# Kernel optimization log

Measured on AMD Instinct MI355X. Metric: run time of the kernel, lower is better.

## Reference

```python
import jax, jax.numpy as jnp
import numpy as np

NF = 512      # nfeatures (input == hidden size)
NL = 3        # nlabels
T = 32768     # sequence length (unbatched)
EPS = 1e-5


def _lstm_layer(x, w_ih, w_hh, b_ih, b_hh):
    # x: [T, F_in]; w_ih: [4H, F_in]; w_hh: [4H, H]
    H = w_hh.shape[1]
    xg = x @ w_ih.T + (b_ih + b_hh)  # precompute input gates: [T, 4H]

    def step(carry, xg_t):
        h, c = carry
        g = xg_t + h @ w_hh.T
        i, f, gc, o = jnp.split(g, 4)
        i = jax.nn.sigmoid(i)
        f = jax.nn.sigmoid(f)
        gc = jnp.tanh(gc)
        o = jax.nn.sigmoid(o)
        c = f * c + i * gc
        h = o * jnp.tanh(c)
        return (h, c), h

    h0 = jnp.zeros((H,), x.dtype)
    _, hs = jax.lax.scan(step, (h0, h0), xg)
    return hs  # [T, H]


def _bn(x, gamma, beta):
    # training-mode BatchNorm1d over the batch (time) axis, biased variance
    m = x.mean(0)
    v = x.var(0)
    return (x - m) * jax.lax.rsqrt(v + EPS) * gamma + beta


def setup_inputs() -> dict:
    key = jax.random.key(0)
    ks = jax.random.split(key, 16)
    s = 1.0 / np.sqrt(NF)
    u = lambda k, shp, sc: jax.random.uniform(k, shp, jnp.float32, -sc, sc)
    inp = {"x": jax.random.normal(ks[0], (T, NF), jnp.float32)}
    # LSTM layer 0 and 1 (input = hidden = NF)
    inp["w_ih0"] = u(ks[1], (4 * NF, NF), s); inp["w_hh0"] = u(ks[2], (4 * NF, NF), s)
    inp["b_ih0"] = u(ks[3], (4 * NF,), s);   inp["b_hh0"] = u(ks[4], (4 * NF,), s)
    inp["w_ih1"] = u(ks[5], (4 * NF, NF), s); inp["w_hh1"] = u(ks[6], (4 * NF, NF), s)
    inp["b_ih1"] = u(ks[7], (4 * NF,), s);   inp["b_hh1"] = u(ks[8], (4 * NF,), s)
    # MLP head
    inp["w1"] = u(ks[9], (128, NF), s);  inp["b1"] = u(ks[9], (128,), s)
    inp["g1"] = jnp.ones((128,), jnp.float32); inp["beta1"] = jnp.zeros((128,), jnp.float32)
    s2 = 1.0 / np.sqrt(128)
    inp["w2"] = u(ks[10], (64, 128), s2); inp["b2"] = u(ks[10], (64,), s2)
    inp["g2"] = jnp.ones((64,), jnp.float32); inp["beta2"] = jnp.zeros((64,), jnp.float32)
    s3 = 1.0 / np.sqrt(64)
    inp["w3"] = u(ks[11], (NL, 64), s3); inp["b3"] = u(ks[11], (NL,), s3)
    return inp


def reference(x, w_ih0, w_hh0, b_ih0, b_hh0, w_ih1, w_hh1, b_ih1, b_hh1,
              w1, b1, g1, beta1, w2, b2, g2, beta2, w3, b3):
    h = _lstm_layer(x, w_ih0, w_hh0, b_ih0, b_hh0)
    h = _lstm_layer(h, w_ih1, w_hh1, b_ih1, b_hh1)
    h = _bn(jax.nn.relu(h @ w1.T + b1), g1, beta1)
    h = _bn(jax.nn.relu(h @ w2.T + b2), g2, beta2)
    return h @ w3.T + b3  # [T, NL]


if __name__ == "__main__":
    out = reference(**setup_inputs())
    print(out.shape, out.dtype)
```

## Files before the change

### kernel.cpp

```cpp
#include <hip/hip_runtime.h>
#include <stdint.h>

#define TSEQ 32768
#define HDIM 512
#define NWGL 64
#define DPW  8
#define POISON32 0x7FA55A5Au

__device__ __forceinline__ float sigf(float x){ return 1.f/(1.f+__expf(-x)); }
__device__ __forceinline__ float tanhf_fast(float x){ return 1.f - 2.f/(1.f+__expf(2.f*x)); }

__device__ __forceinline__ uint32_t agload(uint32_t* p){
  return __hip_atomic_load(p, __ATOMIC_RELAXED, __HIP_MEMORY_SCOPE_AGENT);
}
__device__ __forceinline__ void agstore(uint32_t* p, uint32_t v){
  __hip_atomic_store(p, v, __ATOMIC_RELAXED, __HIP_MEMORY_SCOPE_AGENT);
}

__global__ __launch_bounds__(256,1)
void poison_kernel(uint64_t* __restrict__ a, uint64_t* __restrict__ b, int n64){
  const uint64_t P = (((uint64_t)POISON32)<<32) | (uint64_t)POISON32;
  int i = blockIdx.x*256 + threadIdx.x;
  const int st = gridDim.x*256;
  for (; i < n64; i += st){
    __hip_atomic_store(a+i, P, __ATOMIC_RELAXED, __HIP_MEMORY_SCOPE_AGENT);
    __hip_atomic_store(b+i, P, __ATOMIC_RELAXED, __HIP_MEMORY_SCOPE_AGENT);
  }
}

__global__ __launch_bounds__(256,1)
void lstm_persistent(const float* __restrict__ x,
                     const float* __restrict__ wih0, const float* __restrict__ whh0,
                     const float* __restrict__ bih0, const float* __restrict__ bhh0,
                     const float* __restrict__ wih1, const float* __restrict__ whh1,
                     const float* __restrict__ bih1, const float* __restrict__ bhh1,
                     float* __restrict__ hs0, float* __restrict__ hs1)
{
  const int wg    = blockIdx.x;
  const int layer = (wg >= NWGL) ? 1 : 0;
  const int wgl   = layer ? wg - NWGL : wg;
  const int tid   = threadIdx.x;
  const int r     = tid & 31;
  const int c     = tid >> 5;

  const float* Wih = layer ? wih1 : wih0;
  const float* Whh = layer ? whh1 : whh0;
  float* dst = layer ? hs1 : hs0;

  const int grow = (r>>3)*HDIM + wgl*DPW + (r&7);

  float4 wi[16], wr[16];
  #pragma unroll
  for (int q=0;q<16;q++){
    wi[q] = *(const float4*)&Wih[(size_t)grow*HDIM + c*64 + q*4];
    wr[q] = *(const float4*)&Whh[(size_t)grow*HDIM + c*64 + q*4];
  }
  float bias = 0.f;
  if (tid < 32) bias = (layer?bih1:bih0)[grow] + (layer?bhh1:bhh0)[grow];

  float cstate = 0.f;

  __shared__ float ha[HDIM];
  __shared__ float hr[HDIM];
  __shared__ float part[128];
  __shared__ float gl[32];

  float4 xpref = make_float4(0.f,0.f,0.f,0.f);
  if (!layer && tid >= 128) xpref = *(const float4*)&x[(tid-128)*4];

  #pragma unroll 1
  for (int t = 0; t < TSEQ; ++t){
    if (!layer && tid >= 128) *(float4*)&ha[(tid-128)*4] = xpref;

    if (t > 0 && tid < 128){
      uint32_t* p = (uint32_t*)(dst + (size_t)(t-1)*HDIM) + tid*4;
      uint32_t v0,v1,v2,v3;
      do {
        v0 = agload(p+0); v1 = agload(p+1); v2 = agload(p+2); v3 = agload(p+3);
      } while ((v0==POISON32)|(v1==POISON32)|(v2==POISON32)|(v3==POISON32));
      float4 f; f.x=__uint_as_float(v0); f.y=__uint_as_float(v1);
                f.z=__uint_as_float(v2); f.w=__uint_as_float(v3);
      *(float4*)&hr[tid*4] = f;
    }
    if (layer && tid >= 128){
      uint32_t* p = (uint32_t*)(hs0 + (size_t)t*HDIM) + (tid-128)*4;
      uint32_t v0,v1,v2,v3;
      do {
        v0 = agload(p+0); v1 = agload(p+1); v2 = agload(p+2); v3 = agload(p+3);
      } while ((v0==POISON32)|(v1==POISON32)|(v2==POISON32)|(v3==POISON32));
      float4 f; f.x=__uint_as_float(v0); f.y=__uint_as_float(v1);
                f.z=__uint_as_float(v2); f.w=__uint_as_float(v3);
      *(float4*)&ha[(tid-128)*4] = f;
    }
    if (t == 0 && tid < 128) *(float4*)&hr[tid*4] = make_float4(0.f,0.f,0.f,0.f);
    __syncthreads();

    if (!layer && tid >= 128 && (t+1) < TSEQ)
      xpref = *(const float4*)&x[(size_t)(t+1)*HDIM + (tid-128)*4];

    float s0=0.f,s1=0.f,s2=0.f,s3=0.f;
    const float4* hr4 = (const float4*)(hr + c*64);
    const float4* ha4 = (const float4*)(ha + c*64);
    #pragma unroll
    for (int q=0;q<16;q++){
      float4 hv = hr4[q];
      s0 = fmaf(wr[q].x, hv.x, s0); s1 = fmaf(wr[q].y, hv.y, s1);
      s2 = fmaf(wr[q].z, hv.z, s2); s3 = fmaf(wr[q].w, hv.w, s3);
      float4 av = ha4[q];
      s0 = fmaf(wi[q].x, av.x, s0); s1 = fmaf(wi[q].y, av.y, s1);
      s2 = fmaf(wi[q].z, av.z, s2); s3 = fmaf(wi[q].w, av.w, s3);
    }
    float acc = (s0+s1)+(s2+s3);
    acc += __shfl_xor(acc, 32);
    if ((tid & 63) < 32) part[(tid>>6)*32 + (tid&31)] = acc;
    __syncthreads();
    if (tid < 32) gl[tid] = part[tid] + part[32+tid] + part[64+tid] + part[96+tid] + bias;
    __syncthreads();
    if (tid < 8){
      float gi = sigf(gl[tid]);
      float gf = sigf(gl[8+tid]);
      float gg = tanhf_fast(gl[16+tid]);
      float go = sigf(gl[24+tid]);
      cstate = fmaf(gf, cstate, gi*gg);
      float h = go * tanhf_fast(cstate);
      agstore((uint32_t*)(dst + (size_t)t*HDIM + wgl*DPW + tid), __float_as_uint(h));
    }
  }
}

__global__ __launch_bounds__(256)
void transpose_kernel(const float* __restrict__ w1, const float* __restrict__ w2,
                      float* __restrict__ w1t, float* __restrict__ w2t){
  int i = blockIdx.x*256 + threadIdx.x;
  if (i < 128*512){ int rr = i >> 9, k = i & 511; w1t[k*128 + rr] = w1[i]; }
  if (i < 64*128){ int rr = i >> 7, k = i & 127; w2t[k*64 + rr] = w2[i]; }
}

__global__ __launch_bounds__(128)
void mlp1_kernel(const float* __restrict__ hs1, const float* __restrict__ w1t,
                 const float* __restrict__ b1, float* __restrict__ z1){
  __shared__ float hsl[2048];
  const int tid = threadIdx.x;
  const size_t row0 = (size_t)blockIdx.x*4;
  #pragma unroll
  for (int q=0;q<4;q++){
    int idx = tid + q*128;
    *(float4*)&hsl[idx*4] = *(const float4*)&hs1[row0*512 + idx*4];
  }
  __syncthreads();
  float a0=0.f,a1=0.f,a2=0.f,a3=0.f;
  #pragma unroll 4
  for (int k=0;k<512;k++){
    float wv = w1t[k*128 + tid];
    a0 = fmaf(wv, hsl[k],      a0);
    a1 = fmaf(wv, hsl[512+k],  a1);
    a2 = fmaf(wv, hsl[1024+k], a2);
    a3 = fmaf(wv, hsl[1536+k], a3);
  }
  float bb = b1[tid];
  z1[(row0+0)*128 + tid] = fmaxf(a0+bb, 0.f);
  z1[(row0+1)*128 + tid] = fmaxf(a1+bb, 0.f);
  z1[(row0+2)*128 + tid] = fmaxf(a2+bb, 0.f);
  z1[(row0+3)*128 + tid] = fmaxf(a3+bb, 0.f);
}

template<int NF_>
__global__ void stats_partial(const float* __restrict__ z, float* __restrict__ part){
  const int cf = threadIdx.x;
  const int b  = blockIdx.x;
  float s=0.f, sq=0.f;
  const float* p = z + (size_t)b*512*NF_ + cf;
  for (int rr=0; rr<512; rr++){
    float v = p[(size_t)rr*NF_];
    s += v; sq = fmaf(v, v, sq);
  }
  part[(b*NF_ + cf)*2+0] = s;
  part[(b*NF_ + cf)*2+1] = sq;
}

template<int NF_>
__global__ void stats_final(const float* __restrict__ part, const float* __restrict__ gamma,
                            const float* __restrict__ beta, float* __restrict__ sc,
                            float* __restrict__ sh){
  const int cf = threadIdx.x;
  float s=0.f, sq=0.f;
  for (int b=0;b<64;b++){ s += part[(b*NF_+cf)*2]; sq += part[(b*NF_+cf)*2+1]; }
  const float inv = 1.f/32768.f;
  float m = s*inv;
  float v = fmaf(sq, inv, -m*m);
  float scale = gamma[cf]*rsqrtf(v + 1e-5f);
  sc[cf] = scale;
  sh[cf] = fmaf(-m, scale, beta[cf]);
}

__global__ __launch_bounds__(64)
void mlp2_kernel(const float* __restrict__ z1, const float* __restrict__ w2t,
                 const float* __restrict__ b2, const float* __restrict__ sc1,
                 const float* __restrict__ sh1, float* __restrict__ z2){
  __shared__ float zl[1024];
  const int tid = threadIdx.x;
  const size_t row0 = (size_t)blockIdx.x*8;
  #pragma unroll
  for (int q=0;q<4;q++){
    int idx = tid + q*64;
    float4 v = *(const float4*)&z1[row0*128 + idx*4];
    int k0 = (idx*4) & 127;
    v.x = fmaf(v.x, sc1[k0+0], sh1[k0+0]);
    v.y = fmaf(v.y, sc1[k0+1], sh1[k0+1]);
    v.z = fmaf(v.z, sc1[k0+2], sh1[k0+2]);
    v.w = fmaf(v.w, sc1[k0+3], sh1[k0+3]);
    *(float4*)&zl[idx*4] = v;
  }
  __syncthreads();
  float acc[8] = {0.f,0.f,0.f,0.f,0.f,0.f,0.f,0.f};
  #pragma unroll 4
  for (int k=0;k<128;k++){
    float wv = w2t[k*64 + tid];
    #pragma unroll
    for (int rr=0;rr<8;rr++) acc[rr] = fmaf(wv, zl[rr*128 + k], acc[rr]);
  }
  float bb = b2[tid];
  #pragma unroll
  for (int rr=0;rr<8;rr++)
    z2[(row0+rr)*64 + tid] = fmaxf(acc[rr]+bb, 0.f);
}

__global__ __launch_bounds__(256)
void mlp3_kernel(const float* __restrict__ z2, const float* __restrict__ w3,
                 const float* __restrict__ b3, const float* __restrict__ sc2,
                 const float* __restrict__ sh2, float* __restrict__ out){
  const int tid = threadIdx.x;
  const int lane = tid & 63;
  const size_t row = (size_t)blockIdx.x*4 + (tid>>6);
  float v = fmaf(z2[row*64 + lane], sc2[lane], sh2[lane]);
  float p0 = v*w3[lane], p1 = v*w3[64+lane], p2 = v*w3[128+lane];
  #pragma unroll
  for (int off=32; off; off>>=1){
    p0 += __shfl_xor(p0, off);
    p1 += __shfl_xor(p1, off);
    p2 += __shfl_xor(p2, off);
  }
  if (lane == 0){
    out[row*3+0] = p0 + b3[0];
    out[row*3+1] = p1 + b3[1];
    out[row*3+2] = p2 + b3[2];
  }
}

extern "C" void kernel_launch(void* const* d_in, const int* in_sizes, int n_in,
                              void* d_out, int out_size, void* d_ws, size_t ws_size,
                              hipStream_t stream){
  (void)in_sizes; (void)n_in; (void)out_size;
  const float* x    = (const float*)d_in[0];
  const float* wih0 = (const float*)d_in[1];
  const float* whh0 = (const float*)d_in[2];
  const float* bih0 = (const float*)d_in[3];
  const float* bhh0 = (const float*)d_in[4];
  const float* wih1 = (const float*)d_in[5];
  const float* whh1 = (const float*)d_in[6];
  const float* bih1 = (const float*)d_in[7];
  const float* bhh1 = (const float*)d_in[8];
  const float* w1   = (const float*)d_in[9];
  const float* b1   = (const float*)d_in[10];
  const float* g1   = (const float*)d_in[11];
  const float* be1  = (const float*)d_in[12];
  const float* w2   = (const float*)d_in[13];
  const float* b2   = (const float*)d_in[14];
  const float* g2   = (const float*)d_in[15];
  const float* be2  = (const float*)d_in[16];
  const float* w3   = (const float*)d_in[17];
  const float* b3   = (const float*)d_in[18];
  float* ws  = (float*)d_ws;
  float* out = (float*)d_out;

  if (ws_size < (size_t)33554432ull*4ull) return;

  float* hs0  = ws;
  float* hs1  = ws + 16777216;
  float* z1    = ws;
  float* z2    = ws + 4194304;
  float* w1t   = ws + 6291456;
  float* w2t   = ws + 6356992;
  float* part1 = ws + 6365184;
  float* part2 = ws + 6381568;
  float* sc1   = ws + 6389760;
  float* sh1   = sc1 + 128;
  float* sc2   = sh1 + 128;
  float* sh2   = sc2 + 64;

  poison_kernel<<<1024, 256, 0, stream>>>((uint64_t*)hs0, (uint64_t*)hs1, 8388608);
  lstm_persistent<<<128, 256, 0, stream>>>(x, wih0, whh0, bih0, bhh0,
                                           wih1, whh1, bih1, bhh1, hs0, hs1);
  transpose_kernel<<<256, 256, 0, stream>>>(w1, w2, w1t, w2t);
  mlp1_kernel<<<8192, 128, 0, stream>>>(hs1, w1t, b1, z1);
  stats_partial<128><<<64, 128, 0, stream>>>(z1, part1);
  stats_final<128><<<1, 128, 0, stream>>>(part1, g1, be1, sc1, sh1);
  mlp2_kernel<<<4096, 64, 0, stream>>>(z1, w2t, b2, sc1, sh1, z2);
  stats_partial<64><<<64, 64, 0, stream>>>(z2, part2);
  stats_final<64><<<1, 64, 0, stream>>>(part2, g2, be2, sc2, sh2);
  mlp3_kernel<<<8192, 256, 0, stream>>>(z2, w3, b3, sc2, sh2, out);
}
```

Measured before the change: 75.66 ms.

## Restructure persistent LSTM: 512-thread WGs, bf16 hidden exchange, shuffle gate reduction

Halves the LSTM workgroup count to 32 per layer with 512 threads each, 16 hidden units per workgroup. Hidden states are exchanged between workgroups as packed bf16 pairs through 64-bit atomic polls, and the gate reduction moves from LDS passes to wave shuffles. Double-buffered, swizzled LDS lets the input-weight matvec overlap the recurrent poll. This cuts per-step barriers and inter-CU traffic on the latency-bound recurrence, but rounding hidden states to bf16 lowers precision through both layers and into the MLP head.

```diff
diff --git a/kernel.cpp b/kernel.cpp
--- a/kernel.cpp
+++ b/kernel.cpp
@@ -3,127 +3,176 @@
 
 #define TSEQ 32768
 #define HDIM 512
-#define NWGL 64
-#define DPW  8
-#define POISON32 0x7FA55A5Au
+#define NWGL 32
+#define WGT  512
+#define DPW  16
+#define POISON32 0x7FA57FA5u
+
+typedef float f4 __attribute__((ext_vector_type(4)));
 
 __device__ __forceinline__ float sigf(float x){ return 1.f/(1.f+__expf(-x)); }
 __device__ __forceinline__ float tanhf_fast(float x){ return 1.f - 2.f/(1.f+__expf(2.f*x)); }
 
-__device__ __forceinline__ uint32_t agload(uint32_t* p){
+__device__ __forceinline__ uint64_t agload64(const uint64_t* p){
   return __hip_atomic_load(p, __ATOMIC_RELAXED, __HIP_MEMORY_SCOPE_AGENT);
 }
-__device__ __forceinline__ void agstore(uint32_t* p, uint32_t v){
+__device__ __forceinline__ void agstore32(uint32_t* p, uint32_t v){
   __hip_atomic_store(p, v, __ATOMIC_RELAXED, __HIP_MEMORY_SCOPE_AGENT);
 }
+__device__ __forceinline__ uint32_t f2bf(float f){
+  uint32_t u = __float_as_uint(f);
+  u += 0x7fffu + ((u>>16)&1u);
+  return u>>16;
+}
+__device__ __forceinline__ bool pois(uint64_t v){
+  return (((uint32_t)v)==POISON32) | (((uint32_t)(v>>32))==POISON32);
+}
+__device__ __forceinline__ void unpack_store(uint64_t v, float* buf, int gsw){
+  uint32_t aa = (uint32_t)v, bb = (uint32_t)(v>>32);
+  float4 f;
+  f.x = __uint_as_float(aa<<16);
+  f.y = __uint_as_float(aa & 0xffff0000u);
+  f.z = __uint_as_float(bb<<16);
+  f.w = __uint_as_float(bb & 0xffff0000u);
+  *(float4*)&buf[gsw*4] = f;
+}
+__device__ __forceinline__ f4 ntload(const float* p){
+  return __builtin_nontemporal_load((const f4*)p);
+}
+
+#define PIN4(v) asm volatile("" : "+v"((v).x), "+v"((v).y), "+v"((v).z), "+v"((v).w))
+#define PINS do { _Pragma("unroll") for (int _q=0;_q<16;_q++){ PIN4(wi[_q]); PIN4(wr[_q]); } } while(0)
+
+#define MV(bufptr, W) do { \
+  const float* _b = (bufptr); \
+  _Pragma("unroll") \
+  for (int q=0;q<16;q++){ \
+    float4 hv = *(const float4*)&_b[(((c<<4)|((q^c)&15))<<2)]; \
+    s0 = fmaf(W[q].x, hv.x, s0); s1 = fmaf(W[q].y, hv.y, s1); \
+    s2 = fmaf(W[q].z, hv.z, s2); s3 = fmaf(W[q].w, hv.w, s3); } \
+} while(0)
+
+#define REDUCE_GATES_PUBLISH(dstp) do { \
+  float s = (s0+s1)+(s2+s3); \
+  s += __shfl_xor(s,1); s += __shfl_xor(s,2); s += __shfl_xor(s,4); \
+  s += bias; \
+  float fv = __shfl_down(s,8), gv = __shfl_down(s,16), ov = __shfl_down(s,24); \
+  float gi = sigf(s), gf = sigf(fv), gg = tanhf_fast(gv), go = sigf(ov); \
+  cst = fmaf(gf, cst, gi*gg); \
+  float h = go * tanhf_fast(cst); \
+  float ho = __shfl(h, 32); \
+  if (lane == 0) agstore32((dstp) + (size_t)t*256 + wgl*8 + w, f2bf(h) | (f2bf(ho)<<16)); \
+} while(0)
 
 __global__ __launch_bounds__(256,1)
-void poison_kernel(uint64_t* __restrict__ a, uint64_t* __restrict__ b, int n64){
-  const uint64_t P = (((uint64_t)POISON32)<<32) | (uint64_t)POISON32;
+void poison_kernel(uint64_t* __restrict__ a, int n64){
+  const uint64_t P = 0x7FA57FA57FA57FA5ull;
   int i = blockIdx.x*256 + threadIdx.x;
   const int st = gridDim.x*256;
-  for (; i < n64; i += st){
+  for (; i < n64; i += st)
     __hip_atomic_store(a+i, P, __ATOMIC_RELAXED, __HIP_MEMORY_SCOPE_AGENT);
-    __hip_atomic_store(b+i, P, __ATOMIC_RELAXED, __HIP_MEMORY_SCOPE_AGENT);
-  }
-}
-
-__global__ __launch_bounds__(256,1)
+}
+
+__global__ __launch_bounds__(WGT, 2)
 void lstm_persistent(const float* __restrict__ x,
                      const float* __restrict__ wih0, const float* __restrict__ whh0,
                      const float* __restrict__ bih0, const float* __restrict__ bhh0,
                      const float* __restrict__ wih1, const float* __restrict__ whh1,
                      const float* __restrict__ bih1, const float* __restrict__ bhh1,
-                     float* __restrict__ hs0, float* __restrict__ hs1)
+                     uint32_t* __restrict__ hs0u, uint32_t* __restrict__ hs1u)
 {
   const int wg    = blockIdx.x;
   const int layer = (wg >= NWGL) ? 1 : 0;
   const int wgl   = layer ? wg - NWGL : wg;
   const int tid   = threadIdx.x;
-  const int r     = tid & 31;
-  const int c     = tid >> 5;
+  const int w     = tid >> 6;
+  const int lane  = tid & 63;
+  const int rl    = lane >> 3;
+  const int c     = lane & 7;
+  const int g     = rl & 3;
+  const int dd    = rl >> 2;
+  const int grow  = g*HDIM + wgl*DPW + 2*w + dd;
 
   const float* Wih = layer ? wih1 : wih0;
   const float* Whh = layer ? whh1 : whh0;
-  float* dst = layer ? hs1 : hs0;
-
-  const int grow = (r>>3)*HDIM + wgl*DPW + (r&7);
+  const float bias = (layer?bih1:bih0)[grow] + (layer?bhh1:bhh0)[grow];
 
   float4 wi[16], wr[16];
-  #pragma unroll
-  for (int q=0;q<16;q++){
-    wi[q] = *(const float4*)&Wih[(size_t)grow*HDIM + c*64 + q*4];
-    wr[q] = *(const float4*)&Whh[(size_t)grow*HDIM + c*64 + q*4];
-  }
-  float bias = 0.f;
-  if (tid < 32) bias = (layer?bih1:bih0)[grow] + (layer?bhh1:bhh0)[grow];
-
-  float cstate = 0.f;
-
-  __shared__ float ha[HDIM];
-  __shared__ float hr[HDIM];
-  __shared__ float part[128];
-  __shared__ float gl[32];
-
-  float4 xpref = make_float4(0.f,0.f,0.f,0.f);
-  if (!layer && tid >= 128) xpref = *(const float4*)&x[(tid-128)*4];
-
-  #pragma unroll 1
-  for (int t = 0; t < TSEQ; ++t){
-    if (!layer && tid >= 128) *(float4*)&ha[(tid-128)*4] = xpref;
-
-    if (t > 0 && tid < 128){
-      uint32_t* p = (uint32_t*)(dst + (size_t)(t-1)*HDIM) + tid*4;
-      uint32_t v0,v1,v2,v3;
-      do {
-        v0 = agload(p+0); v1 = agload(p+1); v2 = agload(p+2); v3 = agload(p+3);
-      } while ((v0==POISON32)|(v1==POISON32)|(v2==POISON32)|(v3==POISON32));
-      float4 f; f.x=__uint_as_float(v0); f.y=__uint_as_float(v1);
-                f.z=__uint_as_float(v2); f.w=__uint_as_float(v3);
-      *(float4*)&hr[tid*4] = f;
-    }
-    if (layer && tid >= 128){
-      uint32_t* p = (uint32_t*)(hs0 + (size_t)t*HDIM) + (tid-128)*4;
-      uint32_t v0,v1,v2,v3;
-      do {
-        v0 = agload(p+0); v1 = agload(p+1); v2 = agload(p+2); v3 = agload(p+3);
-      } while ((v0==POISON32)|(v1==POISON32)|(v2==POISON32)|(v3==POISON32));
-      float4 f; f.x=__uint_as_float(v0); f.y=__uint_as_float(v1);
-                f.z=__uint_as_float(v2); f.w=__uint_as_float(v3);
-      *(float4*)&ha[(tid-128)*4] = f;
-    }
-    if (t == 0 && tid < 128) *(float4*)&hr[tid*4] = make_float4(0.f,0.f,0.f,0.f);
-    __syncthreads();
-
-    if (!layer && tid >= 128 && (t+1) < TSEQ)
-      xpref = *(const float4*)&x[(size_t)(t+1)*HDIM + (tid-128)*4];
-
-    float s0=0.f,s1=0.f,s2=0.f,s3=0.f;
-    const float4* hr4 = (const float4*)(hr + c*64);
-    const float4* ha4 = (const float4*)(ha + c*64);
+  {
+    const float* wip = Wih + (size_t)grow*HDIM + c*64;
+    const float* wrp = Whh + (size_t)grow*HDIM + c*64;
     #pragma unroll
     for (int q=0;q<16;q++){
-      float4 hv = hr4[q];
-      s0 = fmaf(wr[q].x, hv.x, s0); s1 = fmaf(wr[q].y, hv.y, s1);
-      s2 = fmaf(wr[q].z, hv.z, s2); s3 = fmaf(wr[q].w, hv.w, s3);
-      float4 av = ha4[q];
-      s0 = fmaf(wi[q].x, av.x, s0); s1 = fmaf(wi[q].y, av.y, s1);
-      s2 = fmaf(wi[q].z, av.z, s2); s3 = fmaf(wi[q].w, av.w, s3);
+      wi[q] = *(const float4*)(wip + 4*q);
+      wr[q] = *(const float4*)(wrp + 4*q);
     }
-    float acc = (s0+s1)+(s2+s3);
-    acc += __shfl_xor(acc, 32);
-    if ((tid & 63) < 32) part[(tid>>6)*32 + (tid&31)] = acc;
+  }
+
+  __shared__ float xab[2][HDIM];
+  __shared__ float hrb[2][HDIM];
+
+  const int t7  = tid & 127;
+  const int gsw = t7 ^ ((t7>>4)&7);
+  float cst = 0.f;
+
+  if (!layer){
+    f4 xnext = (f4){0.f,0.f,0.f,0.f};
+    if (tid < 128){
+      f4 x0 = ntload(x + tid*4);
+      *(f4*)&xab[0][gsw*4] = x0;
+      xnext = ntload(x + HDIM + tid*4);
+      *(f4*)&hrb[0][gsw*4] = (f4){0.f,0.f,0.f,0.f};
+    }
     __syncthreads();
-    if (tid < 32) gl[tid] = part[tid] + part[32+tid] + part[64+tid] + part[96+tid] + bias;
+
+    #pragma unroll 1
+    for (int t = 0; t < TSEQ; ++t){
+      PINS;
+      float s0=0.f,s1=0.f,s2=0.f,s3=0.f;
+      const uint64_t* pp = (const uint64_t*)(hs0u + (size_t)(t-1)*256) + tid;
+      uint64_t v = 0;
+      const bool dp = (t > 0) && (tid < 128);
+      if (dp) v = agload64(pp);
+      MV(&xab[t&1][0], wi);
+      if (tid < 128){
+        *(f4*)&xab[(t+1)&1][gsw*4] = xnext;
+        if (t+2 < TSEQ) xnext = ntload(x + (size_t)(t+2)*HDIM + tid*4);
+        if (t > 0){
+          while (pois(v)) v = agload64(pp);
+          unpack_store(v, &hrb[t&1][0], gsw);
+        }
+      }
+      __syncthreads();
+      MV(&hrb[t&1][0], wr);
+      REDUCE_GATES_PUBLISH(hs0u);
+    }
+  } else {
+    if (tid < 128) *(f4*)&hrb[0][gsw*4] = (f4){0.f,0.f,0.f,0.f};
     __syncthreads();
-    if (tid < 8){
-      float gi = sigf(gl[tid]);
-      float gf = sigf(gl[8+tid]);
-      float gg = tanhf_fast(gl[16+tid]);
-      float go = sigf(gl[24+tid]);
-      cstate = fmaf(gf, cstate, gi*gg);
-      float h = go * tanhf_fast(cstate);
-      agstore((uint32_t*)(dst + (size_t)t*HDIM + wgl*DPW + tid), __float_as_uint(h));
+
+    #pragma unroll 1
+    for (int t = 0; t < TSEQ; ++t){
+      PINS;
+      float s0=0.f,s1=0.f,s2=0.f,s3=0.f;
+      if (tid < 128){
+        const uint64_t* px = (const uint64_t*)(hs0u + (size_t)t*256) + tid;
+        uint64_t v = agload64(px);
+        while (pois(v)) v = agload64(px);
+        unpack_store(v, &xab[t&1][0], gsw);
+      }
+      __syncthreads();
+      const uint64_t* ph = (const uint64_t*)(hs1u + (size_t)(t-1)*256) + tid;
+      uint64_t v2 = 0;
+      const bool dp = (t > 0) && (tid < 128);
+      if (dp) v2 = agload64(ph);
+      MV(&xab[t&1][0], wi);
+      if (dp){
+        while (pois(v2)) v2 = agload64(ph);
+        unpack_store(v2, &hrb[t&1][0], gsw);
+      }
+      __syncthreads();
+      MV(&hrb[t&1][0], wr);
+      REDUCE_GATES_PUBLISH(hs1u);
     }
   }
 }
@@ -137,15 +186,21 @@
 }
 
 __global__ __launch_bounds__(128)
-void mlp1_kernel(const float* __restrict__ hs1, const float* __restrict__ w1t,
+void mlp1_kernel(const uint32_t* __restrict__ hs1u, const float* __restrict__ w1t,
                  const float* __restrict__ b1, float* __restrict__ z1){
   __shared__ float hsl[2048];
   const int tid = threadIdx.x;
   const size_t row0 = (size_t)blockIdx.x*4;
+  const uint4* src = (const uint4*)(hs1u + row0*256);
   #pragma unroll
-  for (int q=0;q<4;q++){
-    int idx = tid + q*128;
-    *(float4*)&hsl[idx*4] = *(const float4*)&hs1[row0*512 + idx*4];
+  for (int q=0;q<2;q++){
+    int j = tid + q*128;
+    uint4 u = src[j];
+    int base = j*8;
+    hsl[base+0] = __uint_as_float(u.x<<16); hsl[base+1] = __uint_as_float(u.x & 0xffff0000u);
+    hsl[base+2] = __uint_as_float(u.y<<16); hsl[base+3] = __uint_as_float(u.y & 0xffff0000u);
+    hsl[base+4] = __uint_as_float(u.z<<16); hsl[base+5] = __uint_as_float(u.z & 0xffff0000u);
+    hsl[base+6] = __uint_as_float(u.w<<16); hsl[base+7] = __uint_as_float(u.w & 0xffff0000u);
   }
   __syncthreads();
   float a0=0.f,a1=0.f,a2=0.f,a3=0.f;
@@ -270,29 +325,29 @@
   const float* be2  = (const float*)d_in[16];
   const float* w3   = (const float*)d_in[17];
   const float* b3   = (const float*)d_in[18];
-  float* ws  = (float*)d_ws;
   float* out = (float*)d_out;
 
-  if (ws_size < (size_t)33554432ull*4ull) return;
-
-  float* hs0  = ws;
-  float* hs1  = ws + 16777216;
-  float* z1    = ws;
-  float* z2    = ws + 4194304;
-  float* w1t   = ws + 6291456;
-  float* w2t   = ws + 6356992;
-  float* part1 = ws + 6365184;
-  float* part2 = ws + 6381568;
-  float* sc1   = ws + 6389760;
+  if (ws_size < (size_t)(96u<<20)) return;
+
+  uint8_t* wb = (uint8_t*)d_ws;
+  uint32_t* hs0u = (uint32_t*)wb;
+  uint32_t* hs1u = (uint32_t*)(wb + (size_t)(32u<<20));
+  float* z1    = (float*)(wb + (size_t)(64u<<20));
+  float* z2    = (float*)(wb + (size_t)(80u<<20));
+  float* w1t   = (float*)(wb + (size_t)(88u<<20));
+  float* w2t   = w1t + 65536;
+  float* part1 = w2t + 8192;
+  float* part2 = part1 + 16384;
+  float* sc1   = part2 + 8192;
   float* sh1   = sc1 + 128;
   float* sc2   = sh1 + 128;
   float* sh2   = sc2 + 64;
 
-  poison_kernel<<<1024, 256, 0, stream>>>((uint64_t*)hs0, (uint64_t*)hs1, 8388608);
-  lstm_persistent<<<128, 256, 0, stream>>>(x, wih0, whh0, bih0, bhh0,
-                                           wih1, whh1, bih1, bhh1, hs0, hs1);
+  poison_kernel<<<1024, 256, 0, stream>>>((uint64_t*)wb, 8*1024*1024);
   transpose_kernel<<<256, 256, 0, stream>>>(w1, w2, w1t, w2t);
-  mlp1_kernel<<<8192, 128, 0, stream>>>(hs1, w1t, b1, z1);
+  lstm_persistent<<<2*NWGL, WGT, 0, stream>>>(x, wih0, whh0, bih0, bhh0,
+                                              wih1, whh1, bih1, bhh1, hs0u, hs1u);
+  mlp1_kernel<<<8192, 128, 0, stream>>>(hs1u, w1t, b1, z1);
   stats_partial<128><<<64, 128, 0, stream>>>(z1, part1);
   stats_final<128><<<1, 128, 0, stream>>>(part1, g1, be1, sc1, sh1);
   mlp2_kernel<<<4096, 64, 0, stream>>>(z1, w2t, b2, sc1, sh1, z2);
```

Measured after the change: 238.5 ms. 215% more time.
